# Kernel optimization log

Measured on AMD Instinct MI355X. Metric: run time of the kernel, lower is better.

Reference implementation:

```python
import jax, jax.numpy as jnp
import numpy as np

N = 100000
F_IN = 128
HID = 16
C = 16
E = 3200000


def setup_inputs() -> dict:
    key = jax.random.key(0)
    k1, k2, k3, k4, k5, k6 = jax.random.split(key, 6)
    x = jax.random.normal(k1, (N, F_IN), dtype=jnp.float32)
    edge_index = jax.random.randint(k2, (2, E), 0, N, dtype=jnp.int64)
    # GCNConv weight (glorot) + bias
    W1 = jax.random.normal(k3, (F_IN, HID), dtype=jnp.float32) * (1.0 / np.sqrt(F_IN))
    b1 = jnp.zeros((HID,), dtype=jnp.float32)
    # pooling linear
    Wp = jax.random.normal(k4, (HID, C), dtype=jnp.float32) * (1.0 / np.sqrt(HID))
    bp = jax.random.normal(k5, (C,), dtype=jnp.float32) * 0.01
    return {"x": x, "W1": W1, "b1": b1, "Wp": Wp, "bp": bp, "edge_index": edge_index}


def gcn_conv(x, W, b, edge_index, num_nodes):
    # PyG GCNConv: add self-loops, symmetric normalization D^-1/2 (A+I) D^-1/2
    loop = jnp.arange(num_nodes, dtype=edge_index.dtype)
    src = jnp.concatenate([edge_index[0], loop])
    dst = jnp.concatenate([edge_index[1], loop])
    ones = jnp.ones_like(dst, dtype=x.dtype)
    deg = jax.ops.segment_sum(ones, dst, num_segments=num_nodes)  # [N]
    dinv = jnp.where(deg > 0, jax.lax.rsqrt(deg), 0.0)
    norm = dinv[src] * dinv[dst]  # [E+N]
    h = x @ W  # [N, HID] transform before aggregation (fewer bytes moved)
    msgs = h[src] * norm[:, None]  # gather + scale
    agg = jax.ops.segment_sum(msgs, dst, num_segments=num_nodes)  # scatter-add
    return agg + b


def reference(x, W1, b1, Wp, bp, edge_index):
    h = jax.nn.relu(gcn_conv(x, W1, b1, edge_index, N))  # [N, HID]
    s = jax.nn.softmax(h @ Wp + bp, axis=1)  # [N, C]
    return s
```

## Files before the change

### kernel.cpp

```cpp
#include <hip/hip_runtime.h>


#define PCHUNK 4096
#define SPLITS 4
#define ACH 2048

__device__ __forceinline__ float bf2f(unsigned int u16) {
    return __uint_as_float(u16 << 16);
}
__device__ __forceinline__ unsigned short f2bf(float f) {
    unsigned int u = __float_as_uint(f);
    u += 0x7fffu + ((u >> 16) & 1u);
    return (unsigned short)(u >> 16);
}

__device__ __forceinline__ void atomAddF(float* p, float v) {
    unsafeAtomicAdd(p, v);
}

__device__ __forceinline__ int voteBf16(const unsigned int* xw, int tid, int* scratch) {
    if (tid == 0) *scratch = 0;
    __syncthreads();
    unsigned int w = xw[tid];
    unsigned int lo = w & 0xffffu;
    unsigned int elo = (lo >> 7) & 0xffu;
    if (lo == 0u || (elo >= 100u && elo <= 140u)) atomicAdd(scratch, 1);
    __syncthreads();
    return (*scratch >= 160) ? 1 : 0;
}

__global__ __launch_bounds__(256) void k_part(const int* __restrict__ ei,
                                              int* __restrict__ cursor,
                                              unsigned int* __restrict__ bkt,
                                              int E, int Nn, int NB, int cap) {
    __shared__ int lhist[512];
    __shared__ int lexcl[512];
    __shared__ int lbase[512];
    __shared__ int sa[512], sb[512];
    __shared__ unsigned int stage[PCHUNK];
    __shared__ ushort sbk[PCHUNK];
    __shared__ int stot_s;
    __shared__ int v64_s;
    int tid = threadIdx.x;
    lhist[tid] = 0; lhist[tid + 256] = 0;
    if (tid == 0) v64_s = 0;
    __syncthreads();
    if (((const unsigned int*)ei)[2 * tid + 1] != 0u) atomicAdd(&v64_s, 1);
    __syncthreads();
    int is64 = (v64_s == 0) ? 1 : 0;
    int e0 = blockIdx.x * PCHUNK;
    int ss[16], dd[16];
    #pragma unroll
    for (int i = 0; i < 16; ++i) {
        int e = e0 + i * 256 + tid;
        int s = -1, d = -1;
        if (e < E) {
            if (is64) { s = ei[2 * e]; d = ei[2 * (E + e)]; }
            else      { s = ei[e];     d = ei[E + e]; }
            if ((unsigned)s >= (unsigned)Nn || (unsigned)d >= (unsigned)Nn) { s = -1; d = -1; }
        }
        ss[i] = s;
        if (d >= 0) {
            int r = atomicAdd(&lhist[d >> 8], 1);
            dd[i] = d | (r << 17);
        } else dd[i] = -1;
    }
    __syncthreads();
    sa[tid] = lhist[tid]; sa[tid + 256] = lhist[tid + 256];
    __syncthreads();
    int* cur = sa; int* nxt = sb;
    for (int off = 1; off < 512; off <<= 1) {
        nxt[tid] = cur[tid] + ((tid >= off) ? cur[tid - off] : 0);
        int t2 = tid + 256;
        nxt[t2] = cur[t2] + ((t2 >= off) ? cur[t2 - off] : 0);
        __syncthreads();
        int* t = cur; cur = nxt; nxt = t;
    }
    lexcl[tid] = cur[tid] - lhist[tid];
    lexcl[tid + 256] = cur[tid + 256] - lhist[tid + 256];
    if (tid == 0) stot_s = cur[511];
    __syncthreads();
    for (int b = tid; b < 512; b += 256) {
        int c = lhist[b];
        if (b < NB && c > 0) {
            int base = atomicAdd(&cursor[b], c);
            lbase[b] = b * cap + base - lexcl[b];
        } else lbase[b] = 0;
    }
    __syncthreads();
    #pragma unroll
    for (int i = 0; i < 16; ++i) {
        if (dd[i] >= 0) {
            int d = dd[i] & 0x1ffff;
            int b = d >> 8;
            int q = lexcl[b] + (dd[i] >> 17);
            stage[q] = (unsigned)ss[i] | ((unsigned)(d & 255) << 17);
            sbk[q] = (ushort)b;
        }
    }
    __syncthreads();
    int stot = stot_s;
    for (int q = tid; q < stot; q += 256) {
        int b = sbk[q];
        int pos = lbase[b] + q;
        if (pos < (b + 1) * cap) bkt[pos] = stage[q];
    }
}

__global__ __launch_bounds__(256) void k_gemmD(const void* __restrict__ xraw,
                                               const void* __restrict__ w1raw,
                                               const unsigned int* __restrict__ bkt,
                                               const int* __restrict__ cursor,
                                               float* __restrict__ dinv,
                                               float* __restrict__ hs,
                                               float* __restrict__ agg,
                                               int Nn, int cap) {
    __shared__ float sWt[16 * 132];
    __shared__ int ldeg[256];
    __shared__ float sdv[256];
    __shared__ int vote_s;
    const ushort* xb = (const ushort*)xraw;
    const float* xf = (const float*)xraw;
    int tid = threadIdx.x, b = blockIdx.x;
    const int isbf = voteBf16((const unsigned int*)xraw, tid, &vote_s);
    ldeg[tid] = 0;
    if (isbf) {
        const ushort* w1 = (const ushort*)w1raw;
        for (int i = tid; i < 2048; i += 256) {
            int k = i >> 4, j = i & 15;
            sWt[j * 132 + k] = bf2f(w1[i]);
        }
    } else {
        const float* w1 = (const float*)w1raw;
        for (int i = tid; i < 2048; i += 256) {
            int k = i >> 4, j = i & 15;
            sWt[j * 132 + k] = w1[i];
        }
    }
    __syncthreads();
    int len = min(cursor[b], cap);
    int bb = b * cap;
    for (int e = tid; e < len; e += 256)
        atomicAdd(&ldeg[(bkt[bb + e] >> 17) & 255u], 1);
    __syncthreads();
    {
        float dv = rsqrtf((float)(ldeg[tid] + 1));
        sdv[tid] = dv;
        int n = (b << 8) + tid;
        if (n < Nn) dinv[n] = dv;
    }
    __syncthreads();
    int hq = tid & 3;
    int nodeq = tid >> 2;
    int n0 = (b << 8) + nodeq * 4;
    float acc[4][4] = {};
    for (int ko = 0; ko < 16; ++ko) {
        float xv[4][8];
        #pragma unroll
        for (int r = 0; r < 4; ++r) {
            int n = n0 + r;
            if (n < Nn) {
                if (isbf) {
                    uint4 q = *reinterpret_cast<const uint4*>(xb + (size_t)n * 128 + ko * 8);
                    xv[r][0] = bf2f(q.x & 0xffffu); xv[r][1] = bf2f(q.x >> 16);
                    xv[r][2] = bf2f(q.y & 0xffffu); xv[r][3] = bf2f(q.y >> 16);
                    xv[r][4] = bf2f(q.z & 0xffffu); xv[r][5] = bf2f(q.z >> 16);
                    xv[r][6] = bf2f(q.w & 0xffffu); xv[r][7] = bf2f(q.w >> 16);
                } else {
                    const float4* p = reinterpret_cast<const float4*>(xf + (size_t)n * 128 + ko * 8);
                    float4 a = p[0], bf = p[1];
                    xv[r][0] = a.x; xv[r][1] = a.y; xv[r][2] = a.z; xv[r][3] = a.w;
                    xv[r][4] = bf.x; xv[r][5] = bf.y; xv[r][6] = bf.z; xv[r][7] = bf.w;
                }
            } else {
                #pragma unroll
                for (int u = 0; u < 8; ++u) xv[r][u] = 0.f;
            }
        }
        #pragma unroll
        for (int c = 0; c < 4; ++c) {
            const float* wr = &sWt[(hq * 4 + c) * 132 + ko * 8];
            float4 w0 = *reinterpret_cast<const float4*>(wr);
            float4 w1v = *reinterpret_cast<const float4*>(wr + 4);
            #pragma unroll
            for (int r = 0; r < 4; ++r) {
                acc[r][c] += xv[r][0] * w0.x + xv[r][1] * w0.y + xv[r][2] * w0.z + xv[r][3] * w0.w
                           + xv[r][4] * w1v.x + xv[r][5] * w1v.y + xv[r][6] * w1v.z + xv[r][7] * w1v.w;
            }
        }
    }
    #pragma unroll
    for (int r = 0; r < 4; ++r) {
        int n = n0 + r;
        if (n < Nn) {
            float dv = sdv[nodeq * 4 + r];
            float4 o = make_float4(acc[r][0] * dv, acc[r][1] * dv, acc[r][2] * dv, acc[r][3] * dv);
            *reinterpret_cast<float4*>(hs + (size_t)n * 16 + hq * 4) = o;
            *reinterpret_cast<float4*>(agg + (size_t)n * 16 + hq * 4) = o;
        }
    }
}

__global__ __launch_bounds__(256) void k_aggS(const unsigned int* __restrict__ bkt,
                                              const int* __restrict__ cursor,
                                              const float* __restrict__ hs,
                                              float* __restrict__ agg, int Nn, int cap) {
    __shared__ float sAgg[4096];
    __shared__ unsigned int sSorted[ACH];
    __shared__ int cnt[256], excl[256];
    __shared__ int sc[2][256];
    __shared__ int tot_s;
    int tid = threadIdx.x;
    int b = blockIdx.x >> 2, sp = blockIdx.x & 3;
    for (int i = tid; i < 4096; i += 256) sAgg[i] = 0.f;
    int len = min(cursor[b], cap);
    int bb = b * cap;
    int s0 = (int)(((long long)len * sp) >> 2);
    int s1 = (int)(((long long)len * (sp + 1)) >> 2);
    int g = tid >> 4, j = tid & 15;
    for (int c0 = s0; c0 < s1; c0 += ACH) {
        cnt[tid] = 0;
        __syncthreads();
        unsigned ue[8];
        int rr[8];
        #pragma unroll
        for (int i = 0; i < 8; ++i) {
            int idx = c0 + i * 256 + tid;
            if (idx < s1) {
                ue[i] = bkt[bb + idx];
                rr[i] = atomicAdd(&cnt[(ue[i] >> 17) & 255u], 1);
            } else { ue[i] = 0xffffffffu; rr[i] = 0; }
        }
        __syncthreads();
        int v = cnt[tid];
        sc[0][tid] = v;
        __syncthreads();
        int pi = 0;
        for (int off = 1; off < 256; off <<= 1) {
            sc[pi ^ 1][tid] = sc[pi][tid] + ((tid >= off) ? sc[pi][tid - off] : 0);
            __syncthreads();
            pi ^= 1;
        }
        excl[tid] = sc[pi][tid] - v;
        if (tid == 255) tot_s = sc[pi][255];
        __syncthreads();
        #pragma unroll
        for (int i = 0; i < 8; ++i) {
            if (ue[i] != 0xffffffffu)
                sSorted[excl[(ue[i] >> 17) & 255u] + rr[i]] = ue[i];
        }
        __syncthreads();
        #pragma unroll 2
        for (int nn = 0; nn < 16; ++nn) {
            int node = g * 16 + nn;
            int segS = excl[node];
            int segE = (node == 255) ? tot_s : excl[node + 1];
            float acc = 0.f;
            #pragma unroll 1
            for (int base = segS; base < segE; base += 8) {
                int m = segE - base;
                unsigned e8[8];
                float vv[8];
                #pragma unroll
                for (int i = 0; i < 8; ++i) {
                    int idx = base + i;
                    e8[i] = sSorted[(idx < segE) ? idx : segS];
                }
                #pragma unroll
                for (int i = 0; i < 8; ++i)
                    vv[i] = hs[(size_t)(e8[i] & 0x1ffffu) * 16 + j];
                #pragma unroll
                for (int i = 0; i < 8; ++i)
                    vv[i] = (i < m) ? vv[i] : 0.f;
                vv[0] += vv[4]; vv[1] += vv[5]; vv[2] += vv[6]; vv[3] += vv[7];
                vv[0] += vv[2]; vv[1] += vv[3];
                acc += vv[0] + vv[1];
            }
            if (segE > segS) sAgg[node * 16 + j] += acc;
        }
        __syncthreads();
    }
    int nbase = b << 8;
    for (int i = tid; i < 4096; i += 256) {
        int n = nbase + (i >> 4);
        float v = sAgg[i];
        bool nz = (n < Nn) && (v != 0.f);
        if (__any(nz)) {
            if (n < Nn) atomAddF(&agg[(size_t)n * 16 + (i & 15)], v);
        }
    }
}

__global__ __launch_bounds__(256) void k_final(const float* __restrict__ agg,
                                               const float* __restrict__ dinv,
                                               const void* __restrict__ xraw,
                                               const void* __restrict__ b1raw,
                                               const void* __restrict__ wpraw,
                                               const void* __restrict__ bpraw,
                                               void* __restrict__ outraw, int Nn) {
    __shared__ float sWp[256];
    __shared__ float sA[256];
    __shared__ int vote_s;
    int tid = threadIdx.x;
    const int isbf = voteBf16((const unsigned int*)xraw, tid, &vote_s);
    sWp[tid] = isbf ? bf2f(((const ushort*)wpraw)[tid]) : ((const float*)wpraw)[tid];
    int n0 = blockIdx.x * 16;
    int nl = tid >> 4, c = tid & 15;
    int n = n0 + nl;
    float b1v = isbf ? bf2f(((const ushort*)b1raw)[c]) : ((const float*)b1raw)[c];
    float bpv = isbf ? bf2f(((const ushort*)bpraw)[c]) : ((const float*)bpraw)[c];
    float av = (n < Nn) ? agg[(size_t)n * 16 + c] * dinv[n] : 0.f;
    sA[tid] = fmaxf(av + b1v, 0.f);
    __syncthreads();
    float acc = bpv;
    #pragma unroll
    for (int jj = 0; jj < 16; ++jj) acc += sA[nl * 16 + jj] * sWp[jj * 16 + c];
    float m = acc;
    #pragma unroll
    for (int off = 1; off < 16; off <<= 1) m = fmaxf(m, __shfl_xor(m, off, 16));
    float ev = __expf(acc - m);
    float s = ev;
    #pragma unroll
    for (int off = 1; off < 16; off <<= 1) s += __shfl_xor(s, off, 16);
    if (n < Nn) {
        float v = ev / s;
        if (isbf) ((ushort*)outraw)[(size_t)n * 16 + c] = f2bf(v);
        else      ((float*)outraw)[(size_t)n * 16 + c] = v;
    }
}

extern "C" void kernel_launch(void* const* d_in, const int* in_sizes, int n_in,
                              void* d_out, int out_size, void* d_ws, size_t ws_size,
                              hipStream_t stream) {
    const void* x  = d_in[0];
    const void* W1 = d_in[1];
    const void* b1 = d_in[2];
    const void* Wp = d_in[3];
    const void* bp = d_in[4];
    const int*  ei = (const int*)d_in[5];

    int Nn = in_sizes[0] / 128;
    int E  = in_sizes[5] / 2;
    int NB = (Nn + 255) >> 8;

    size_t Ns = (size_t)Nn;
    char* ws = (char*)d_ws;
    size_t off = 0;
    auto alloc = [&](size_t bytes) { void* p = ws + off; off += (bytes + 63) & ~(size_t)63; return p; };
    float* hs     = (float*)alloc(Ns * 16 * 4);
    float* agg    = (float*)alloc(Ns * 16 * 4);
    float* dinv   = (float*)alloc(Ns * 4);
    int*   cursor = (int*)alloc(512 * 4);
    size_t remain = (ws_size > off) ? (ws_size - off) : 0;
    int cap = (int)(remain / 4 / (size_t)NB);
    int want = 12288;
    if (cap > want) cap = want;
    cap &= ~63;
    unsigned int* bkt = (unsigned int*)alloc((size_t)NB * (size_t)cap * 4);

    hipMemsetAsync(cursor, 0, 512 * 4, stream);
    k_part<<<(E + PCHUNK - 1) / PCHUNK, 256, 0, stream>>>(ei, cursor, bkt, E, Nn, NB, cap);
    k_gemmD<<<NB, 256, 0, stream>>>(x, W1, bkt, cursor, dinv, hs, agg, Nn, cap);
    k_aggS<<<NB * SPLITS, 256, 0, stream>>>(bkt, cursor, hs, agg, Nn, cap);
    k_final<<<(Nn + 15) / 16, 256, 0, stream>>>(agg, dinv, x, b1, Wp, bp, d_out, Nn);
}
```

Before: 243.1 us.

## Halve destination buckets and fuse aggregation with final softmax kernel

Destination buckets shrink from 256 to 128 nodes, so each aggregation block owns a whole bucket. That removes the 4-way split, the global float atomics into agg and the agg buffer itself. The epilogue (self-loop add, dinv scaling, bias, ReLU, pooling linear, softmax) now runs inside the aggregation kernel, which drops one kernel launch and one round trip of the N×16 array through memory. The cost is fewer aggregation blocks (782 instead of 1564), with more edges processed serially per block. The partition kernel also does a larger 1024-entry scan.

```diff
diff --git a/kernel.cpp b/kernel.cpp
--- a/kernel.cpp
+++ b/kernel.cpp
@@ -2,7 +2,6 @@
 
 
 #define PCHUNK 4096
-#define SPLITS 4
 #define ACH 2048
 
 __device__ __forceinline__ float bf2f(unsigned int u16) {
@@ -14,10 +13,6 @@
     return (unsigned short)(u >> 16);
 }
 
-__device__ __forceinline__ void atomAddF(float* p, float v) {
-    unsafeAtomicAdd(p, v);
-}
-
 __device__ __forceinline__ int voteBf16(const unsigned int* xw, int tid, int* scratch) {
     if (tid == 0) *scratch = 0;
     __syncthreads();
@@ -32,17 +27,18 @@
 __global__ __launch_bounds__(256) void k_part(const int* __restrict__ ei,
                                               int* __restrict__ cursor,
                                               unsigned int* __restrict__ bkt,
-                                              int E, int Nn, int NB, int cap) {
-    __shared__ int lhist[512];
-    __shared__ int lexcl[512];
-    __shared__ int lbase[512];
-    __shared__ int sa[512], sb[512];
+                                              int E, int Nn, int NB2, int cap) {
+    __shared__ int lhist[1024];
+    __shared__ int lexcl[1024];
+    __shared__ int lbase[1024];
+    __shared__ int sa[1024], sb[1024];
     __shared__ unsigned int stage[PCHUNK];
     __shared__ ushort sbk[PCHUNK];
     __shared__ int stot_s;
     __shared__ int v64_s;
     int tid = threadIdx.x;
-    lhist[tid] = 0; lhist[tid + 256] = 0;
+    #pragma unroll
+    for (int k = 0; k < 4; ++k) lhist[tid + k * 256] = 0;
     if (tid == 0) v64_s = 0;
     __syncthreads();
     if (((const unsigned int*)ei)[2 * tid + 1] != 0u) atomicAdd(&v64_s, 1);
@@ -61,28 +57,34 @@
         }
         ss[i] = s;
         if (d >= 0) {
-            int r = atomicAdd(&lhist[d >> 8], 1);
+            int r = atomicAdd(&lhist[d >> 7], 1);
             dd[i] = d | (r << 17);
         } else dd[i] = -1;
     }
     __syncthreads();
-    sa[tid] = lhist[tid]; sa[tid + 256] = lhist[tid + 256];
+    #pragma unroll
+    for (int k = 0; k < 4; ++k) sa[tid + k * 256] = lhist[tid + k * 256];
     __syncthreads();
     int* cur = sa; int* nxt = sb;
-    for (int off = 1; off < 512; off <<= 1) {
-        nxt[tid] = cur[tid] + ((tid >= off) ? cur[tid - off] : 0);
-        int t2 = tid + 256;
-        nxt[t2] = cur[t2] + ((t2 >= off) ? cur[t2 - off] : 0);
+    for (int off = 1; off < 1024; off <<= 1) {
+        #pragma unroll
+        for (int k = 0; k < 4; ++k) {
+            int i = tid + k * 256;
+            nxt[i] = cur[i] + ((i >= off) ? cur[i - off] : 0);
+        }
         __syncthreads();
         int* t = cur; cur = nxt; nxt = t;
     }
-    lexcl[tid] = cur[tid] - lhist[tid];
-    lexcl[tid + 256] = cur[tid + 256] - lhist[tid + 256];
-    if (tid == 0) stot_s = cur[511];
-    __syncthreads();
-    for (int b = tid; b < 512; b += 256) {
+    #pragma unroll
+    for (int k = 0; k < 4; ++k) {
+        int i = tid + k * 256;
+        lexcl[i] = cur[i] - lhist[i];
+    }
+    if (tid == 0) stot_s = cur[1023];
+    __syncthreads();
+    for (int b = tid; b < 1024; b += 256) {
         int c = lhist[b];
-        if (b < NB && c > 0) {
+        if (b < NB2 && c > 0) {
             int base = atomicAdd(&cursor[b], c);
             lbase[b] = b * cap + base - lexcl[b];
         } else lbase[b] = 0;
@@ -92,9 +94,9 @@
     for (int i = 0; i < 16; ++i) {
         if (dd[i] >= 0) {
             int d = dd[i] & 0x1ffff;
-            int b = d >> 8;
+            int b = d >> 7;
             int q = lexcl[b] + (dd[i] >> 17);
-            stage[q] = (unsigned)ss[i] | ((unsigned)(d & 255) << 17);
+            stage[q] = (unsigned)ss[i] | ((unsigned)(d & 127) << 17);
             sbk[q] = (ushort)b;
         }
     }
@@ -113,8 +115,7 @@
                                                const int* __restrict__ cursor,
                                                float* __restrict__ dinv,
                                                float* __restrict__ hs,
-                                               float* __restrict__ agg,
-                                               int Nn, int cap) {
+                                               int Nn, int NB2, int cap) {
     __shared__ float sWt[16 * 132];
     __shared__ int ldeg[256];
     __shared__ float sdv[256];
@@ -138,10 +139,18 @@
         }
     }
     __syncthreads();
-    int len = min(cursor[b], cap);
-    int bb = b * cap;
-    for (int e = tid; e < len; e += 256)
-        atomicAdd(&ldeg[(bkt[bb + e] >> 17) & 255u], 1);
+    {
+        int b0 = 2 * b;
+        int len0 = (b0 < NB2) ? min(cursor[b0], cap) : 0;
+        size_t bb0 = (size_t)b0 * cap;
+        for (int e = tid; e < len0; e += 256)
+            atomicAdd(&ldeg[(bkt[bb0 + e] >> 17) & 127u], 1);
+        int b1i = 2 * b + 1;
+        int len1 = (b1i < NB2) ? min(cursor[b1i], cap) : 0;
+        size_t bb1 = (size_t)b1i * cap;
+        for (int e = tid; e < len1; e += 256)
+            atomicAdd(&ldeg[128 + ((bkt[bb1 + e] >> 17) & 127u)], 1);
+    }
     __syncthreads();
     {
         float dv = rsqrtf((float)(ldeg[tid] + 1));
@@ -196,65 +205,72 @@
             float dv = sdv[nodeq * 4 + r];
             float4 o = make_float4(acc[r][0] * dv, acc[r][1] * dv, acc[r][2] * dv, acc[r][3] * dv);
             *reinterpret_cast<float4*>(hs + (size_t)n * 16 + hq * 4) = o;
-            *reinterpret_cast<float4*>(agg + (size_t)n * 16 + hq * 4) = o;
-        }
-    }
-}
-
-__global__ __launch_bounds__(256) void k_aggS(const unsigned int* __restrict__ bkt,
+        }
+    }
+}
+
+__global__ __launch_bounds__(256) void k_aggF(const unsigned int* __restrict__ bkt,
                                               const int* __restrict__ cursor,
                                               const float* __restrict__ hs,
-                                              float* __restrict__ agg, int Nn, int cap) {
-    __shared__ float sAgg[4096];
+                                              const float* __restrict__ dinv,
+                                              const void* __restrict__ xraw,
+                                              const void* __restrict__ b1raw,
+                                              const void* __restrict__ wpraw,
+                                              const void* __restrict__ bpraw,
+                                              void* __restrict__ outraw,
+                                              int Nn, int cap) {
+    __shared__ float sAgg[2048];
     __shared__ unsigned int sSorted[ACH];
-    __shared__ int cnt[256], excl[256];
-    __shared__ int sc[2][256];
-    __shared__ int tot_s;
-    int tid = threadIdx.x;
-    int b = blockIdx.x >> 2, sp = blockIdx.x & 3;
-    for (int i = tid; i < 4096; i += 256) sAgg[i] = 0.f;
+    __shared__ int cnt[128], excl[128];
+    __shared__ int sc[2][128];
+    __shared__ float sWp[256];
+    __shared__ float sA[256];
+    __shared__ int tot_s, vote_s;
+    int tid = threadIdx.x, b = blockIdx.x;
+    const int isbf = voteBf16((const unsigned int*)xraw, tid, &vote_s);
+    sWp[tid] = isbf ? bf2f(((const ushort*)wpraw)[tid]) : ((const float*)wpraw)[tid];
+    for (int i = tid; i < 2048; i += 256) sAgg[i] = 0.f;
     int len = min(cursor[b], cap);
-    int bb = b * cap;
-    int s0 = (int)(((long long)len * sp) >> 2);
-    int s1 = (int)(((long long)len * (sp + 1)) >> 2);
+    size_t bb = (size_t)b * cap;
     int g = tid >> 4, j = tid & 15;
-    for (int c0 = s0; c0 < s1; c0 += ACH) {
-        cnt[tid] = 0;
+    for (int c0 = 0; c0 < len; c0 += ACH) {
+        if (tid < 128) cnt[tid] = 0;
         __syncthreads();
         unsigned ue[8];
         int rr[8];
         #pragma unroll
         for (int i = 0; i < 8; ++i) {
             int idx = c0 + i * 256 + tid;
-            if (idx < s1) {
+            if (idx < len) {
                 ue[i] = bkt[bb + idx];
-                rr[i] = atomicAdd(&cnt[(ue[i] >> 17) & 255u], 1);
+                rr[i] = atomicAdd(&cnt[(ue[i] >> 17) & 127u], 1);
             } else { ue[i] = 0xffffffffu; rr[i] = 0; }
         }
         __syncthreads();
-        int v = cnt[tid];
-        sc[0][tid] = v;
+        int v = (tid < 128) ? cnt[tid] : 0;
+        if (tid < 128) sc[0][tid] = v;
         __syncthreads();
         int pi = 0;
-        for (int off = 1; off < 256; off <<= 1) {
-            sc[pi ^ 1][tid] = sc[pi][tid] + ((tid >= off) ? sc[pi][tid - off] : 0);
+        for (int off = 1; off < 128; off <<= 1) {
+            if (tid < 128) sc[pi ^ 1][tid] = sc[pi][tid] + ((tid >= off) ? sc[pi][tid - off] : 0);
             __syncthreads();
             pi ^= 1;
         }
-        excl[tid] = sc[pi][tid] - v;
-        if (tid == 255) tot_s = sc[pi][255];
+        if (tid < 128) excl[tid] = sc[pi][tid] - v;
+        if (tid == 127) tot_s = sc[pi][127];
         __syncthreads();
         #pragma unroll
         for (int i = 0; i < 8; ++i) {
             if (ue[i] != 0xffffffffu)
-                sSorted[excl[(ue[i] >> 17) & 255u] + rr[i]] = ue[i];
-        }
-        __syncthreads();
+                sSorted[excl[(ue[i] >> 17) & 127u] + rr[i]] = ue[i];
+        }
+        __syncthreads();
+        int tot = tot_s;
         #pragma unroll 2
-        for (int nn = 0; nn < 16; ++nn) {
-            int node = g * 16 + nn;
+        for (int nn = 0; nn < 8; ++nn) {
+            int node = g * 8 + nn;
             int segS = excl[node];
-            int segE = (node == 255) ? tot_s : excl[node + 1];
+            int segE = (node == 127) ? tot : excl[node + 1];
             float acc = 0.f;
             #pragma unroll 1
             for (int base = segS; base < segE; base += 8) {
@@ -280,52 +296,36 @@
         }
         __syncthreads();
     }
-    int nbase = b << 8;
-    for (int i = tid; i < 4096; i += 256) {
-        int n = nbase + (i >> 4);
-        float v = sAgg[i];
-        bool nz = (n < Nn) && (v != 0.f);
-        if (__any(nz)) {
-            if (n < Nn) atomAddF(&agg[(size_t)n * 16 + (i & 15)], v);
-        }
-    }
-}
-
-__global__ __launch_bounds__(256) void k_final(const float* __restrict__ agg,
-                                               const float* __restrict__ dinv,
-                                               const void* __restrict__ xraw,
-                                               const void* __restrict__ b1raw,
-                                               const void* __restrict__ wpraw,
-                                               const void* __restrict__ bpraw,
-                                               void* __restrict__ outraw, int Nn) {
-    __shared__ float sWp[256];
-    __shared__ float sA[256];
-    __shared__ int vote_s;
-    int tid = threadIdx.x;
-    const int isbf = voteBf16((const unsigned int*)xraw, tid, &vote_s);
-    sWp[tid] = isbf ? bf2f(((const ushort*)wpraw)[tid]) : ((const float*)wpraw)[tid];
-    int n0 = blockIdx.x * 16;
+    __syncthreads();
     int nl = tid >> 4, c = tid & 15;
-    int n = n0 + nl;
     float b1v = isbf ? bf2f(((const ushort*)b1raw)[c]) : ((const float*)b1raw)[c];
     float bpv = isbf ? bf2f(((const ushort*)bpraw)[c]) : ((const float*)bpraw)[c];
-    float av = (n < Nn) ? agg[(size_t)n * 16 + c] * dinv[n] : 0.f;
-    sA[tid] = fmaxf(av + b1v, 0.f);
-    __syncthreads();
-    float acc = bpv;
-    #pragma unroll
-    for (int jj = 0; jj < 16; ++jj) acc += sA[nl * 16 + jj] * sWp[jj * 16 + c];
-    float m = acc;
-    #pragma unroll
-    for (int off = 1; off < 16; off <<= 1) m = fmaxf(m, __shfl_xor(m, off, 16));
-    float ev = __expf(acc - m);
-    float s = ev;
-    #pragma unroll
-    for (int off = 1; off < 16; off <<= 1) s += __shfl_xor(s, off, 16);
-    if (n < Nn) {
-        float v = ev / s;
-        if (isbf) ((ushort*)outraw)[(size_t)n * 16 + c] = f2bf(v);
-        else      ((float*)outraw)[(size_t)n * 16 + c] = v;
+    int nbase = b << 7;
+    #pragma unroll 1
+    for (int pass = 0; pass < 8; ++pass) {
+        int node = pass * 16 + nl;
+        int n = nbase + node;
+        float dv = 0.f, sv = 0.f;
+        if (n < Nn) { dv = dinv[n]; sv = hs[(size_t)n * 16 + c]; }
+        float hval = fmaxf(dv * (sv + sAgg[node * 16 + c]) + b1v, 0.f);
+        sA[tid] = hval;
+        __syncthreads();
+        float acc = bpv;
+        #pragma unroll
+        for (int jj = 0; jj < 16; ++jj) acc += sA[nl * 16 + jj] * sWp[jj * 16 + c];
+        float m = acc;
+        #pragma unroll
+        for (int off = 1; off < 16; off <<= 1) m = fmaxf(m, __shfl_xor(m, off, 16));
+        float ev = __expf(acc - m);
+        float s = ev;
+        #pragma unroll
+        for (int off = 1; off < 16; off <<= 1) s += __shfl_xor(s, off, 16);
+        if (n < Nn) {
+            float val = ev / s;
+            if (isbf) ((ushort*)outraw)[(size_t)n * 16 + c] = f2bf(val);
+            else      ((float*)outraw)[(size_t)n * 16 + c] = val;
+        }
+        __syncthreads();
     }
 }
 
@@ -339,28 +339,27 @@
     const void* bp = d_in[4];
     const int*  ei = (const int*)d_in[5];
 
-    int Nn = in_sizes[0] / 128;
-    int E  = in_sizes[5] / 2;
-    int NB = (Nn + 255) >> 8;
+    int Nn  = in_sizes[0] / 128;
+    int E   = in_sizes[5] / 2;
+    int NB  = (Nn + 255) >> 8;
+    int NB2 = (Nn + 127) >> 7;
 
     size_t Ns = (size_t)Nn;
     char* ws = (char*)d_ws;
     size_t off = 0;
     auto alloc = [&](size_t bytes) { void* p = ws + off; off += (bytes + 63) & ~(size_t)63; return p; };
     float* hs     = (float*)alloc(Ns * 16 * 4);
-    float* agg    = (float*)alloc(Ns * 16 * 4);
     float* dinv   = (float*)alloc(Ns * 4);
-    int*   cursor = (int*)alloc(512 * 4);
+    int*   cursor = (int*)alloc(1024 * 4);
     size_t remain = (ws_size > off) ? (ws_size - off) : 0;
-    int cap = (int)(remain / 4 / (size_t)NB);
-    int want = 12288;
+    int cap = (int)(remain / 4 / (size_t)NB2);
+    int want = 6144;
     if (cap > want) cap = want;
     cap &= ~63;
-    unsigned int* bkt = (unsigned int*)alloc((size_t)NB * (size_t)cap * 4);
-
-    hipMemsetAsync(cursor, 0, 512 * 4, stream);
-    k_part<<<(E + PCHUNK - 1) / PCHUNK, 256, 0, stream>>>(ei, cursor, bkt, E, Nn, NB, cap);
-    k_gemmD<<<NB, 256, 0, stream>>>(x, W1, bkt, cursor, dinv, hs, agg, Nn, cap);
-    k_aggS<<<NB * SPLITS, 256, 0, stream>>>(bkt, cursor, hs, agg, Nn, cap);
-    k_final<<<(Nn + 15) / 16, 256, 0, stream>>>(agg, dinv, x, b1, Wp, bp, d_out, Nn);
-}
+    unsigned int* bkt = (unsigned int*)alloc((size_t)NB2 * (size_t)cap * 4);
+
+    hipMemsetAsync(cursor, 0, 1024 * 4, stream);
+    k_part<<<(E + PCHUNK - 1) / PCHUNK, 256, 0, stream>>>(ei, cursor, bkt, E, Nn, NB2, cap);
+    k_gemmD<<<NB, 256, 0, stream>>>(x, W1, bkt, cursor, dinv, hs, Nn, NB2, cap);
+    k_aggF<<<NB2, 256, 0, stream>>>(bkt, cursor, hs, dinv, x, b1, Wp, bp, d_out, Nn, cap);
+}
```

New measurement: 251.5 us. 3.5% more time.
